# Performance work log

Measured on AMD Instinct MI355X. Metric: run time of the kernel, lower is better.

The kernel has to match this reference:

```python
import jax, jax.numpy as jnp
import numpy as np

N_HEAD = 16
N_KV_HEAD = 4
HEAD_DIM = 64
ROPE_THETA = 10000.0
EPS = 1e-6


def _rope_cos_sin(T, D, theta):
    # matches torch: freqs_cis[t, i] = exp(1j * t * theta**(-2i/D)), i in [0, D//2)
    inv_freq = theta ** (-jnp.arange(0, D, 2, dtype=jnp.float32) / D)  # [D//2]
    freqs = jnp.arange(T, dtype=jnp.float32)[:, None] * inv_freq[None, :]  # [T, D//2]
    return jnp.cos(freqs), jnp.sin(freqs)


def _apply_rope(x, cos, sin):
    # x: [B, T, H, D]; pairs are (even, odd) along last dim, complex-multiplied by freqs_cis
    B, T, H, D = x.shape
    xr = x.reshape(B, T, H, D // 2, 2)
    xe, xo = xr[..., 0], xr[..., 1]
    c = cos[None, :, None, :]  # [1, T, 1, D//2]
    s = sin[None, :, None, :]
    oe = xe * c - xo * s
    oo = xe * s + xo * c
    return jnp.stack([oe, oo], axis=-1).reshape(B, T, H, D)


def _qk_norm(x):
    rms = jnp.sqrt(jnp.mean(x * x, axis=-1, keepdims=True) + EPS)
    return x / rms


def setup_inputs() -> dict:
    key = jax.random.key(0)
    k = jax.random.split(key, 5)
    B, T, C = 4, 2048, 1024
    sc = 1.0 / np.sqrt(C)
    return {
        "x": jax.random.normal(k[0], (B, T, C), jnp.float32),
        "wq": jax.random.normal(k[1], (N_HEAD * HEAD_DIM, C), jnp.float32) * sc,
        "wk": jax.random.normal(k[2], (N_KV_HEAD * HEAD_DIM, C), jnp.float32) * sc,
        "wv": jax.random.normal(k[3], (N_KV_HEAD * HEAD_DIM, C), jnp.float32) * sc,
        "wo": jax.random.normal(k[4], (C, N_HEAD * HEAD_DIM), jnp.float32) * sc,
    }


def reference(x, wq, wk, wv, wo):
    B, T, C = x.shape
    H, KVH, D = N_HEAD, N_KV_HEAD, HEAD_DIM
    n_rep = H // KVH

    q = (x @ wq.T).reshape(B, T, H, D)
    k = (x @ wk.T).reshape(B, T, KVH, D)
    v = (x @ wv.T).reshape(B, T, KVH, D)

    cos, sin = _rope_cos_sin(T, D, ROPE_THETA)
    q = _qk_norm(_apply_rope(q, cos, sin))
    k = _qk_norm(_apply_rope(k, cos, sin))

    # GQA expand kv heads to n_head
    k = jnp.repeat(k, n_rep, axis=2)  # [B, T, H, D]
    v = jnp.repeat(v, n_rep, axis=2)

    q = q.transpose(0, 2, 1, 3)  # [B, H, T, D]
    k = k.transpose(0, 2, 1, 3)
    v = v.transpose(0, 2, 1, 3)

    scale = 1.0 / np.sqrt(D)
    scores = jnp.einsum("bhqd,bhkd->bhqk", q, k) * scale
    causal = jnp.tril(jnp.ones((T, T), dtype=bool))
    scores = jnp.where(causal[None, None], scores, -jnp.inf)
    attn = jax.nn.softmax(scores, axis=-1)
    y = jnp.einsum("bhqk,bhkd->bhqd", attn, v)  # [B, H, T, D]
    y = y.transpose(0, 2, 1, 3).reshape(B, T, H * D)
    return y @ wo.T
```

## Files before the change

kernel.cpp:

```cpp
#include <hip/hip_runtime.h>
#include <hip/hip_bf16.h>
#include <type_traits>

typedef __attribute__((ext_vector_type(8))) __bf16 bf16x8;
typedef __attribute__((ext_vector_type(2))) float f32x2;
typedef __attribute__((ext_vector_type(4))) float f32x4;
typedef __attribute__((ext_vector_type(16))) float f32x16;

#define MFMA16(a, b, c) __builtin_amdgcn_mfma_f32_16x16x32_bf16((a), (b), (c), 0, 0, 0)
#define MFMA32(a, b, c) __builtin_amdgcn_mfma_f32_32x32x16_bf16((a), (b), (c), 0, 0, 0)

__device__ __forceinline__ unsigned short f2bf(float f) {
    unsigned u = __builtin_bit_cast(unsigned, f);
    u = (u + 0x7fffu + ((u >> 16) & 1u)) >> 16;
    return (unsigned short)u;
}

__device__ __forceinline__ float bf2f(unsigned short u) {
    return __builtin_bit_cast(float, (unsigned)u << 16);
}

__device__ __forceinline__ unsigned cvt_pk_bf16(float lo, float hi) {
    unsigned r;
    asm("v_cvt_pk_bf16_f32 %0, %1, %2" : "=v"(r) : "v"(lo), "v"(hi));
    return r;
}

__device__ __forceinline__ void permswap(unsigned& a, unsigned& b) {
    asm("v_permlane32_swap_b32 %0, %1" : "+v"(a), "+v"(b));
}

__device__ __forceinline__ void gll16(const void* g, void* l) {
    __builtin_amdgcn_global_load_lds((const __attribute__((address_space(1))) void*)g,
                                     (__attribute__((address_space(3))) void*)l, 16, 0, 0);
}

__global__ __launch_bounds__(256) void cvt_fused(const float4* __restrict__ x,
                                                 const float4* __restrict__ wq,
                                                 const float4* __restrict__ wk,
                                                 const float4* __restrict__ wv,
                                                 const float4* __restrict__ wo,
                                                 ushort4* __restrict__ xb,
                                                 ushort4* __restrict__ wqkvb,
                                                 ushort4* __restrict__ wob,
                                                 float2* __restrict__ tbl) {
    int i = blockIdx.x * 256 + threadIdx.x;
    if (i < 2752512) {
        const float4* src; ushort4* dst; int j;
        if (i < 2097152)      { src = x;  dst = xb;             j = i; }
        else if (i < 2359296) { src = wq; dst = wqkvb;          j = i - 2097152; }
        else if (i < 2424832) { src = wk; dst = wqkvb + 262144; j = i - 2359296; }
        else if (i < 2490368) { src = wv; dst = wqkvb + 327680; j = i - 2424832; }
        else                  { src = wo; dst = wob;            j = i - 2490368; }
        float4 v = src[j];
        ushort4 o;
        o.x = f2bf(v.x); o.y = f2bf(v.y); o.z = f2bf(v.z); o.w = f2bf(v.w);
        dst[j] = o;
    } else {
        int j = i - 2752512;
        int t = j >> 5, k = j & 31;
        float inv = powf(10000.0f, -(float)(2 * k) * (1.0f / 64.0f));
        float a = (float)t * inv;
        tbl[j] = make_float2(cosf(a), sinf(a));
    }
}

template <typename OT>
__global__ __launch_bounds__(256) void gemm_bt_t(const unsigned short* __restrict__ A,
                                                 const unsigned short* __restrict__ Bt,
                                                 OT* __restrict__ C, int M, int N, int K) {
    __shared__ unsigned short As[2][128 * 32];
    __shared__ unsigned short Bs[2][128 * 32];
    const int tid = threadIdx.x;
    const int wid = tid >> 6, lane = tid & 63;
    const size_t brow = (size_t)blockIdx.x * 128, bcol = (size_t)blockIdx.y * 128;
    const int nkt = K >> 5;

    auto stage = [&](int buf, int kt) {
#pragma unroll
        for (int j = 0; j < 2; ++j) {
            int e = (j * 256 + tid) * 8;
            int r = e >> 5, c = e & 31;
            gll16(A + (brow + r) * K + kt * 32 + c, &As[buf][e]);
        }
#pragma unroll
        for (int j = 0; j < 2; ++j) {
            int e = (j * 256 + tid) * 8;
            int r = e >> 5, c = e & 31;
            gll16(Bt + (bcol + r) * K + kt * 32 + c, &Bs[buf][e]);
        }
    };

    f32x4 acc[4][4] = {};
    const int wm = (wid >> 1) * 64, wn = (wid & 1) * 64;
    const int fr = lane & 15, fk = (lane >> 4) * 8;

    stage(0, 0);
    for (int kt = 0; kt < nkt; ++kt) {
        __syncthreads();
        if (kt + 1 < nkt) stage((kt + 1) & 1, kt + 1);
        const int buf = kt & 1;
        bf16x8 af[4], bfr[4];
#pragma unroll
        for (int i = 0; i < 4; ++i)
            af[i] = *(const bf16x8*)&As[buf][(wm + i * 16 + fr) * 32 + fk];
#pragma unroll
        for (int i = 0; i < 4; ++i)
            bfr[i] = *(const bf16x8*)&Bs[buf][(wn + i * 16 + fr) * 32 + fk];
#pragma unroll
        for (int i = 0; i < 4; ++i)
#pragma unroll
            for (int j = 0; j < 4; ++j)
                acc[i][j] = MFMA16(af[i], bfr[j], acc[i][j]);
    }

    const int orow = (lane >> 4) * 4, ocol = lane & 15;
#pragma unroll
    for (int i = 0; i < 4; ++i)
#pragma unroll
        for (int j = 0; j < 4; ++j)
#pragma unroll
            for (int r = 0; r < 4; ++r) {
                size_t idx = (brow + wm + i * 16 + orow + r) * N + (bcol + wn + j * 16 + ocol);
                if constexpr (std::is_same_v<OT, unsigned short>)
                    C[idx] = f2bf(acc[i][j][r]);
                else
                    C[idx] = acc[i][j][r];
            }
}

__global__ __launch_bounds__(256) void rope_norm(const unsigned short* __restrict__ qkvb,
                                                 const float2* __restrict__ tbl,
                                                 unsigned short* __restrict__ qb,
                                                 unsigned short* __restrict__ kb) {
    int unit = blockIdx.x * 4 + (threadIdx.x >> 6);
    int lane = threadIdx.x & 63;
    int row = unit / 20;
    int hh = unit - row * 20;
    int b = row >> 11, t = row & 2047;
    int col = (hh < 16) ? hh * 64 : 1024 + (hh - 16) * 64;
    float x = bf2f(qkvb[(size_t)row * 1536 + col + lane]);
    float partner = __shfl_xor(x, 1);
    float2 cs = tbl[t * 32 + (lane >> 1)];
    float sgn = (lane & 1) ? cs.y : -cs.y;
    float o = x * cs.x + partner * sgn;
    float ss = o * o;
#pragma unroll
    for (int off = 1; off < 64; off <<= 1) ss += __shfl_xor(ss, off);
    o = o * rsqrtf(ss * (1.0f / 64.0f) + 1e-6f);
    if (hh < 16) o *= 0.18033688f;
    unsigned short ob = f2bf(o);
    if (hh < 16)
        qb[(((size_t)(b * 16 + hh)) * 2048 + t) * 64 + lane] = ob;
    else
        kb[(((size_t)(b * 4 + (hh - 16))) * 2048 + t) * 64 + lane] = ob;
}

__global__ __launch_bounds__(256) void vtrans(const unsigned short* __restrict__ qkvb,
                                              unsigned short* __restrict__ vt) {
    __shared__ unsigned short tile[64][72];
    int bk = blockIdx.y, t0 = blockIdx.x * 64;
    int b = bk >> 2, kvh = bk & 3;
    int i = threadIdx.x >> 2, c0 = (threadIdx.x & 3) * 16;
    const unsigned short* src = qkvb + ((size_t)(b * 2048 + t0)) * 1536 + 1280 + kvh * 64;
#pragma unroll
    for (int j = 0; j < 16; ++j) tile[i][c0 + j] = src[(size_t)i * 1536 + c0 + j];
    __syncthreads();
    unsigned short* dst = vt + (size_t)bk * 64 * 2048 + (size_t)i * 2048 + t0 + c0;
#pragma unroll
    for (int j = 0; j < 16; ++j) dst[j] = tile[c0 + j][i];
}

__global__ __launch_bounds__(256, 4) void attn_fwd(const unsigned short* __restrict__ qb,
                                                   const unsigned short* __restrict__ kbuf,
                                                   const unsigned short* __restrict__ vt,
                                                   unsigned short* __restrict__ Pp,
                                                   float* __restrict__ Lp) {
    int orig = blockIdx.x;
    int wg = (orig & 7) * 320 + (orig >> 3);
    int bh = wg / 40;
    int u = 39 - (wg - bh * 40);
    int qt, ci, nc;
    if (u < 4)       { qt = u;               ci = 0;            nc = 1; }
    else if (u < 12) { qt = 4 + ((u - 4) >> 1);  ci = (u - 4) & 1;  nc = 2; }
    else if (u < 24) { qt = 8 + (u - 12) / 3;    ci = (u - 12) % 3; nc = 3; }
    else             { qt = 12 + ((u - 24) >> 2); ci = (u - 24) & 3; nc = 4; }
    const int nkt = 2 * qt + 2;
    const int t0 = ci * nkt / nc, t1 = (ci + 1) * nkt / nc;
    const int qbase = qt * 128;

    int b = bh >> 4, h = bh & 15, kvh = h >> 2;
    int tid = threadIdx.x, wid = tid >> 6, lane = tid & 63;
    int qrow0 = qbase + wid * 32;
    const unsigned short* Q = qb + ((size_t)(b * 16 + h)) * 2048 * 64;
    const unsigned short* Kp = kbuf + ((size_t)(b * 4 + kvh)) * 2048 * 64;
    const unsigned short* Vp = vt + ((size_t)(b * 4 + kvh)) * 64 * 2048;
    const int q32 = lane & 31, hi = lane >> 5;
    const int swz = (q32 & 7) ^ ((q32 >> 3) & 3);

    __shared__ unsigned short Klds[2][4096];
    __shared__ unsigned short Vlds[2][4096];

    auto stage = [&](int buf, int kt) {
#pragma unroll
        for (int j = 0; j < 2; ++j) {
            int t = j * 256 + tid;
            int k = t >> 3, c = (t & 7) ^ (k & 7) ^ ((k >> 3) & 3);
            gll16(Kp + ((size_t)(kt * 64 + k)) * 64 + c * 8, &Klds[buf][t * 8]);
        }
#pragma unroll
        for (int j = 0; j < 2; ++j) {
            int t = j * 256 + tid;
            int d = t >> 3, c = (t & 7) ^ (d & 7) ^ ((d >> 3) & 3);
            gll16(Vp + (size_t)d * 2048 + kt * 64 + c * 8, &Vlds[buf][t * 8]);
        }
    };

    bf16x8 qf[4];
#pragma unroll
    for (int kd = 0; kd < 4; ++kd)
        qf[kd] = *(const bf16x8*)&Q[(qrow0 + q32) * 64 + kd * 16 + hi * 8];

    f32x16 accO[2] = {};
    f32x2 lr2 = {0.0f, 0.0f};
    f32x16 s0v;
#pragma unroll
    for (int i = 0; i < 16; ++i) s0v[i] = -11.54156036f;

    stage(0, t0);
    for (int kt = t0; kt < t1; ++kt) {
        __syncthreads();
        if (kt + 1 < t1) stage((kt + 1 - t0) & 1, kt + 1);
        const int cur = (kt - t0) & 1;
        const int kb0 = kt * 64;
        if (kb0 <= qrow0 + 31) {
            const int qg = qrow0 + q32;
            const bool diag = (kb0 + 63 > qrow0);
            bf16x8 pf[4];
#pragma unroll
            for (int j = 0; j < 2; ++j) {
                f32x16 s = s0v;
                const int row = j * 32 + q32;
                __builtin_amdgcn_s_setprio(1);
#pragma unroll
                for (int kd = 0; kd < 4; ++kd) {
                    bf16x8 kf = *(const bf16x8*)&Klds[cur][row * 64 + ((2 * kd + hi) ^ swz) * 8];
                    s = MFMA32(kf, qf[kd], s);
                }
                __builtin_amdgcn_s_setprio(0);
                float p[16];
                if (diag) {
#pragma unroll
                    for (int r = 0; r < 16; ++r) {
                        float v = __builtin_exp2f(s[r]);
                        int key = kb0 + j * 32 + (r & 3) + 8 * (r >> 2) + 4 * hi;
                        if (key > qg) v = 0.0f;
                        p[r] = v;
                    }
                } else {
#pragma unroll
                    for (int r = 0; r < 16; ++r) p[r] = __builtin_exp2f(s[r]);
                }
#pragma unroll
                for (int i = 0; i < 8; ++i) {
                    f32x2 pp = {p[2 * i], p[2 * i + 1]};
                    asm("v_pk_add_f32 %0, %0, %1" : "+v"(lr2) : "v"(pp));
                }
#pragma unroll
                for (int kl = 0; kl < 2; ++kl) {
                    unsigned c0 = cvt_pk_bf16(p[8 * kl + 0], p[8 * kl + 1]);
                    unsigned c1 = cvt_pk_bf16(p[8 * kl + 4], p[8 * kl + 5]);
                    unsigned c2 = cvt_pk_bf16(p[8 * kl + 2], p[8 * kl + 3]);
                    unsigned c3 = cvt_pk_bf16(p[8 * kl + 6], p[8 * kl + 7]);
                    permswap(c0, c1);
                    permswap(c2, c3);
                    union { bf16x8 v; unsigned u[4]; } pk;
                    pk.u[0] = c0; pk.u[1] = c2; pk.u[2] = c1; pk.u[3] = c3;
                    pf[j * 2 + kl] = pk.v;
                }
            }
            __builtin_amdgcn_s_setprio(1);
#pragma unroll
            for (int nd = 0; nd < 2; ++nd) {
                int row = nd * 32 + q32;
#pragma unroll
                for (int ks = 0; ks < 4; ++ks) {
                    bf16x8 vf = *(const bf16x8*)&Vlds[cur][row * 64 + ((2 * ks + hi) ^ swz) * 8];
                    accO[nd] = MFMA32(pf[ks], vf, accO[nd]);
                }
            }
            __builtin_amdgcn_s_setprio(0);
        }
    }

    float lrun = lr2[0] + lr2[1];
    unsigned lu = __builtin_bit_cast(unsigned, lrun);
    unsigned la = lu, lb = lu;
    permswap(la, lb);
    float L = __builtin_bit_cast(float, la) + __builtin_bit_cast(float, lb);

    unsigned short* Pw = Pp + (((size_t)bh * 40 + u) * 128 + wid * 32) * 64;
#pragma unroll
    for (int nd = 0; nd < 2; ++nd)
#pragma unroll
        for (int r = 0; r < 16; ++r) {
            int lrow = (r & 3) + 8 * (r >> 2) + 4 * hi;
            Pw[(size_t)lrow * 64 + nd * 32 + q32] = f2bf(accO[nd][r]);
        }
    if (lane < 32)
        Lp[((size_t)bh * 40 + u) * 128 + wid * 32 + q32] = L;
}

__global__ __launch_bounds__(256) void attn_fin(const unsigned short* __restrict__ Pp,
                                                const float* __restrict__ Lp,
                                                unsigned short* __restrict__ y) {
    int idx = blockIdx.x * 256 + threadIdx.x;
    int dg = idx & 15;
    int grow = idx >> 4;
    int bh = grow >> 11, t = grow & 2047;
    int b = bh >> 4, h = bh & 15;
    int qt = t >> 7;
    int bse, nc;
    if (qt < 4)       { bse = qt;                nc = 1; }
    else if (qt < 8)  { bse = 4 + 2 * (qt - 4);  nc = 2; }
    else if (qt < 12) { bse = 12 + 3 * (qt - 8); nc = 3; }
    else              { bse = 24 + 4 * (qt - 12); nc = 4; }
    float o0 = 0.f, o1 = 0.f, o2 = 0.f, o3 = 0.f, L = 0.f;
    for (int ci = 0; ci < nc; ++ci) {
        size_t slot = ((size_t)bh * 40 + bse + ci) * 128 + (t & 127);
        ushort4 pw = *(const ushort4*)&Pp[slot * 64 + dg * 4];
        o0 += bf2f(pw.x); o1 += bf2f(pw.y); o2 += bf2f(pw.z); o3 += bf2f(pw.w);
        L += Lp[slot];
    }
    float inv = 1.0f / L;
    ushort4 w;
    w.x = f2bf(o0 * inv); w.y = f2bf(o1 * inv);
    w.z = f2bf(o2 * inv); w.w = f2bf(o3 * inv);
    *(ushort4*)&y[((size_t)(b * 2048 + t)) * 1024 + h * 64 + dg * 4] = w;
}

extern "C" void kernel_launch(void* const* d_in, const int* in_sizes, int n_in,
                              void* d_out, int out_size, void* d_ws, size_t ws_size,
                              hipStream_t stream) {
    const float* x = (const float*)d_in[0];
    const float* wq = (const float*)d_in[1];
    const float* wk = (const float*)d_in[2];
    const float* wv = (const float*)d_in[3];
    const float* wo = (const float*)d_in[4];
    float* out = (float*)d_out;

    char* ws = (char*)d_ws;
    size_t off = 0;
    auto alloc = [&](size_t bytes) {
        void* p = ws + off;
        off += (bytes + 255) & ~(size_t)255;
        return p;
    };
    unsigned short* xb    = (unsigned short*)alloc(8192ull * 1024 * 2);
    unsigned short* wqkvb = (unsigned short*)alloc(1536ull * 1024 * 2);
    unsigned short* wob   = (unsigned short*)alloc(1024ull * 1024 * 2);
    char*           big   = (char*)alloc(41943040ull + 1310720ull);
    float2*         tbl   = (float2*)alloc(2048ull * 32 * 8);
    unsigned short* qb    = (unsigned short*)alloc(8192ull * 1024 * 2);
    unsigned short* kb    = (unsigned short*)alloc(4ull * 4 * 2048 * 64 * 2);
    unsigned short* vt    = (unsigned short*)alloc(4ull * 4 * 64 * 2048 * 2);

    unsigned short* qkvb  = (unsigned short*)big;
    unsigned short* Pp    = (unsigned short*)big;
    float*          Lp    = (float*)(big + 41943040ull);
    unsigned short* ybf   = xb;

    cvt_fused<<<11008, 256, 0, stream>>>((const float4*)x, (const float4*)wq, (const float4*)wk,
                                         (const float4*)wv, (const float4*)wo,
                                         (ushort4*)xb, (ushort4*)wqkvb, (ushort4*)wob, tbl);

    gemm_bt_t<unsigned short><<<dim3(64, 12), 256, 0, stream>>>(xb, wqkvb, qkvb, 8192, 1536, 1024);

    rope_norm<<<(8192 * 20) / 4, 256, 0, stream>>>(qkvb, tbl, qb, kb);

    vtrans<<<dim3(32, 16), 256, 0, stream>>>(qkvb, vt);

    attn_fwd<<<2560, 256, 0, stream>>>(qb, kb, vt, Pp, Lp);

    attn_fin<<<8192, 256, 0, stream>>>(Pp, Lp, ybf);

    gemm_bt_t<float><<<dim3(64, 8), 256, 0, stream>>>(ybf, wob, out, 8192, 1024, 1024);
}
```

Baseline: 174.8 us.

## Fuse RoPE, QK-norm and V transpose into QKV GEMM epilogue

Adds a QKV GEMM whose epilogue applies rotary embedding and RMS normalisation in registers and writes Q/K in head-major layout and V transposed. This removes the rope_norm and vtrans kernels and the round trip of the intermediate qkv buffer through memory. Separately, attention staging now precomputes and increments global pointers instead of recomputing addresses, and the row-sum accumulation is split into four independent accumulators to shorten the dependency chain. The epilogue issues many per-element table loads and shuffles and uses scattered 2-byte stores, which may be less coalesced than before.

Result: no change. 174.2 us, median of 4 (-0.4%).

```diff
diff --git a/kernel.cpp b/kernel.cpp
--- a/kernel.cpp
+++ b/kernel.cpp
@@ -65,6 +65,127 @@
     }
 }
 
+__global__ __launch_bounds__(256) void gemm_qkv(const unsigned short* __restrict__ A,
+                                                const unsigned short* __restrict__ Bt,
+                                                const float2* __restrict__ tbl,
+                                                unsigned short* __restrict__ qb,
+                                                unsigned short* __restrict__ kb,
+                                                unsigned short* __restrict__ vt) {
+    const int K = 1024;
+    __shared__ unsigned short As[2][128 * 32];
+    __shared__ unsigned short Bs[2][128 * 32];
+    const int tid = threadIdx.x;
+    const int wid = tid >> 6, lane = tid & 63;
+    const size_t brow = (size_t)blockIdx.x * 128, bcol = (size_t)blockIdx.y * 128;
+    const int nkt = K >> 5;
+
+    auto stage = [&](int buf, int kt) {
+#pragma unroll
+        for (int j = 0; j < 2; ++j) {
+            int e = (j * 256 + tid) * 8;
+            int r = e >> 5, c = e & 31;
+            gll16(A + (brow + r) * K + kt * 32 + c, &As[buf][e]);
+        }
+#pragma unroll
+        for (int j = 0; j < 2; ++j) {
+            int e = (j * 256 + tid) * 8;
+            int r = e >> 5, c = e & 31;
+            gll16(Bt + (bcol + r) * K + kt * 32 + c, &Bs[buf][e]);
+        }
+    };
+
+    f32x4 acc[4][4] = {};
+    const int wm = (wid >> 1) * 64, wn = (wid & 1) * 64;
+    const int fr = lane & 15, fk = (lane >> 4) * 8;
+
+    stage(0, 0);
+    for (int kt = 0; kt < nkt; ++kt) {
+        __syncthreads();
+        if (kt + 1 < nkt) stage((kt + 1) & 1, kt + 1);
+        const int buf = kt & 1;
+        bf16x8 af[4], bfr[4];
+#pragma unroll
+        for (int i = 0; i < 4; ++i)
+            af[i] = *(const bf16x8*)&As[buf][(wm + i * 16 + fr) * 32 + fk];
+#pragma unroll
+        for (int i = 0; i < 4; ++i)
+            bfr[i] = *(const bf16x8*)&Bs[buf][(wn + i * 16 + fr) * 32 + fk];
+#pragma unroll
+        for (int i = 0; i < 4; ++i)
+#pragma unroll
+            for (int j = 0; j < 4; ++j)
+                acc[i][j] = MFMA16(af[i], bfr[j], acc[i][j]);
+    }
+
+    const int orow = (lane >> 4) * 4, ocol = lane & 15;
+    const int tokrow0 = (int)brow + wm;
+    const int hcol0 = (int)bcol + wn;
+
+    if (blockIdx.y < 10) {
+        float ss[4][4];
+#pragma unroll
+        for (int i = 0; i < 4; ++i)
+#pragma unroll
+            for (int r = 0; r < 4; ++r) ss[i][r] = 0.0f;
+#pragma unroll
+        for (int i = 0; i < 4; ++i)
+#pragma unroll
+            for (int j = 0; j < 4; ++j) {
+                const int m = (j * 16 + ocol) >> 1;
+#pragma unroll
+                for (int r = 0; r < 4; ++r) {
+                    float xv = acc[i][j][r];
+                    float partner = __shfl_xor(xv, 1);
+                    int t = (tokrow0 + i * 16 + orow + r) & 2047;
+                    float2 cs = tbl[t * 32 + m];
+                    float sgn = (ocol & 1) ? cs.y : -cs.y;
+                    float v = fmaf(xv, cs.x, partner * sgn);
+                    acc[i][j][r] = v;
+                    ss[i][r] += v * v;
+                }
+            }
+#pragma unroll
+        for (int off = 1; off < 16; off <<= 1)
+#pragma unroll
+            for (int i = 0; i < 4; ++i)
+#pragma unroll
+                for (int r = 0; r < 4; ++r) ss[i][r] += __shfl_xor(ss[i][r], off);
+        const bool isq = (blockIdx.y < 8);
+        const float qsc = isq ? 0.18033688f : 1.0f;
+        const int h = hcol0 >> 6;
+#pragma unroll
+        for (int i = 0; i < 4; ++i)
+#pragma unroll
+            for (int r = 0; r < 4; ++r) {
+                float sc = rsqrtf(ss[i][r] * (1.0f / 64.0f) + 1e-6f) * qsc;
+                int grow = tokrow0 + i * 16 + orow + r;
+                int b = grow >> 11, t = grow & 2047;
+                unsigned short* dst = isq
+                    ? qb + (((size_t)(b * 16 + h)) * 2048 + t) * 64
+                    : kb + (((size_t)(b * 4 + (h - 16))) * 2048 + t) * 64;
+#pragma unroll
+                for (int j = 0; j < 4; ++j)
+                    dst[j * 16 + ocol] = f2bf(acc[i][j][r] * sc);
+            }
+    } else {
+#pragma unroll
+        for (int j = 0; j < 4; ++j) {
+            int vcol = (hcol0 - 1280) + j * 16 + ocol;
+            int kvh = vcol >> 6, d = vcol & 63;
+#pragma unroll
+            for (int i = 0; i < 4; ++i) {
+                int grow = tokrow0 + i * 16 + orow;
+                int b = grow >> 11, t = grow & 2047;
+                ushort4 w;
+#pragma unroll
+                for (int r = 0; r < 4; ++r)
+                    ((unsigned short*)&w)[r] = f2bf(acc[i][j][r]);
+                *(ushort4*)&vt[((size_t)(b * 4 + kvh) * 64 + d) * 2048 + t] = w;
+            }
+        }
+    }
+}
+
 template <typename OT>
 __global__ __launch_bounds__(256) void gemm_bt_t(const unsigned short* __restrict__ A,
                                                  const unsigned short* __restrict__ Bt,
@@ -127,48 +248,6 @@
                 else
                     C[idx] = acc[i][j][r];
             }
-}
-
-__global__ __launch_bounds__(256) void rope_norm(const unsigned short* __restrict__ qkvb,
-                                                 const float2* __restrict__ tbl,
-                                                 unsigned short* __restrict__ qb,
-                                                 unsigned short* __restrict__ kb) {
-    int unit = blockIdx.x * 4 + (threadIdx.x >> 6);
-    int lane = threadIdx.x & 63;
-    int row = unit / 20;
-    int hh = unit - row * 20;
-    int b = row >> 11, t = row & 2047;
-    int col = (hh < 16) ? hh * 64 : 1024 + (hh - 16) * 64;
-    float x = bf2f(qkvb[(size_t)row * 1536 + col + lane]);
-    float partner = __shfl_xor(x, 1);
-    float2 cs = tbl[t * 32 + (lane >> 1)];
-    float sgn = (lane & 1) ? cs.y : -cs.y;
-    float o = x * cs.x + partner * sgn;
-    float ss = o * o;
-#pragma unroll
-    for (int off = 1; off < 64; off <<= 1) ss += __shfl_xor(ss, off);
-    o = o * rsqrtf(ss * (1.0f / 64.0f) + 1e-6f);
-    if (hh < 16) o *= 0.18033688f;
-    unsigned short ob = f2bf(o);
-    if (hh < 16)
-        qb[(((size_t)(b * 16 + hh)) * 2048 + t) * 64 + lane] = ob;
-    else
-        kb[(((size_t)(b * 4 + (hh - 16))) * 2048 + t) * 64 + lane] = ob;
-}
-
-__global__ __launch_bounds__(256) void vtrans(const unsigned short* __restrict__ qkvb,
-                                              unsigned short* __restrict__ vt) {
-    __shared__ unsigned short tile[64][72];
-    int bk = blockIdx.y, t0 = blockIdx.x * 64;
-    int b = bk >> 2, kvh = bk & 3;
-    int i = threadIdx.x >> 2, c0 = (threadIdx.x & 3) * 16;
-    const unsigned short* src = qkvb + ((size_t)(b * 2048 + t0)) * 1536 + 1280 + kvh * 64;
-#pragma unroll
-    for (int j = 0; j < 16; ++j) tile[i][c0 + j] = src[(size_t)i * 1536 + c0 + j];
-    __syncthreads();
-    unsigned short* dst = vt + (size_t)bk * 64 * 2048 + (size_t)i * 2048 + t0 + c0;
-#pragma unroll
-    for (int j = 0; j < 16; ++j) dst[j] = tile[c0 + j][i];
 }
 
 __global__ __launch_bounds__(256, 4) void attn_fwd(const unsigned short* __restrict__ qb,
@@ -201,19 +280,22 @@
     __shared__ unsigned short Klds[2][4096];
     __shared__ unsigned short Vlds[2][4096];
 
-    auto stage = [&](int buf, int kt) {
-#pragma unroll
-        for (int j = 0; j < 2; ++j) {
-            int t = j * 256 + tid;
-            int k = t >> 3, c = (t & 7) ^ (k & 7) ^ ((k >> 3) & 3);
-            gll16(Kp + ((size_t)(kt * 64 + k)) * 64 + c * 8, &Klds[buf][t * 8]);
-        }
-#pragma unroll
-        for (int j = 0; j < 2; ++j) {
-            int t = j * 256 + tid;
-            int d = t >> 3, c = (t & 7) ^ (d & 7) ^ ((d >> 3) & 3);
-            gll16(Vp + (size_t)d * 2048 + kt * 64 + c * 8, &Vlds[buf][t * 8]);
-        }
+    const unsigned short *gk0, *gk1, *gv0, *gv1;
+    {
+        int t = tid, k = t >> 3, c = (t & 7) ^ (k & 7) ^ ((k >> 3) & 3);
+        gk0 = Kp + ((size_t)(t0 * 64 + k)) * 64 + c * 8;
+        t = 256 + tid; k = t >> 3; c = (t & 7) ^ (k & 7) ^ ((k >> 3) & 3);
+        gk1 = Kp + ((size_t)(t0 * 64 + k)) * 64 + c * 8;
+        t = tid; int d = t >> 3; c = (t & 7) ^ (d & 7) ^ ((d >> 3) & 3);
+        gv0 = Vp + (size_t)d * 2048 + t0 * 64 + c * 8;
+        t = 256 + tid; d = t >> 3; c = (t & 7) ^ (d & 7) ^ ((d >> 3) & 3);
+        gv1 = Vp + (size_t)d * 2048 + t0 * 64 + c * 8;
+    }
+    auto stage = [&](int buf) {
+        gll16(gk0, &Klds[buf][tid * 8]);        gk0 += 4096;
+        gll16(gk1, &Klds[buf][2048 + tid * 8]); gk1 += 4096;
+        gll16(gv0, &Vlds[buf][tid * 8]);        gv0 += 64;
+        gll16(gv1, &Vlds[buf][2048 + tid * 8]); gv1 += 64;
     };
 
     bf16x8 qf[4];
@@ -222,15 +304,15 @@
         qf[kd] = *(const bf16x8*)&Q[(qrow0 + q32) * 64 + kd * 16 + hi * 8];
 
     f32x16 accO[2] = {};
-    f32x2 lr2 = {0.0f, 0.0f};
+    f32x2 lra = {0.0f, 0.0f}, lrb = {0.0f, 0.0f}, lrc = {0.0f, 0.0f}, lrd = {0.0f, 0.0f};
     f32x16 s0v;
 #pragma unroll
     for (int i = 0; i < 16; ++i) s0v[i] = -11.54156036f;
 
-    stage(0, t0);
+    stage(0);
     for (int kt = t0; kt < t1; ++kt) {
         __syncthreads();
-        if (kt + 1 < t1) stage((kt + 1 - t0) & 1, kt + 1);
+        if (kt + 1 < t1) stage((kt + 1 - t0) & 1);
         const int cur = (kt - t0) & 1;
         const int kb0 = kt * 64;
         if (kb0 <= qrow0 + 31) {
@@ -261,10 +343,19 @@
 #pragma unroll
                     for (int r = 0; r < 16; ++r) p[r] = __builtin_exp2f(s[r]);
                 }
-#pragma unroll
-                for (int i = 0; i < 8; ++i) {
-                    f32x2 pp = {p[2 * i], p[2 * i + 1]};
-                    asm("v_pk_add_f32 %0, %0, %1" : "+v"(lr2) : "v"(pp));
+                {
+                    f32x2 p0 = {p[0], p[1]},  p1 = {p[2], p[3]};
+                    f32x2 p2 = {p[4], p[5]},  p3 = {p[6], p[7]};
+                    asm("v_pk_add_f32 %0, %0, %1" : "+v"(lra) : "v"(p0));
+                    asm("v_pk_add_f32 %0, %0, %1" : "+v"(lrb) : "v"(p1));
+                    asm("v_pk_add_f32 %0, %0, %1" : "+v"(lrc) : "v"(p2));
+                    asm("v_pk_add_f32 %0, %0, %1" : "+v"(lrd) : "v"(p3));
+                    f32x2 p4 = {p[8], p[9]},  p5 = {p[10], p[11]};
+                    f32x2 p6 = {p[12], p[13]}, p7 = {p[14], p[15]};
+                    asm("v_pk_add_f32 %0, %0, %1" : "+v"(lra) : "v"(p4));
+                    asm("v_pk_add_f32 %0, %0, %1" : "+v"(lrb) : "v"(p5));
+                    asm("v_pk_add_f32 %0, %0, %1" : "+v"(lrc) : "v"(p6));
+                    asm("v_pk_add_f32 %0, %0, %1" : "+v"(lrd) : "v"(p7));
                 }
 #pragma unroll
                 for (int kl = 0; kl < 2; ++kl) {
@@ -293,7 +384,10 @@
         }
     }
 
-    float lrun = lr2[0] + lr2[1];
+    asm("v_pk_add_f32 %0, %0, %1" : "+v"(lra) : "v"(lrc));
+    asm("v_pk_add_f32 %0, %0, %1" : "+v"(lrb) : "v"(lrd));
+    asm("v_pk_add_f32 %0, %0, %1" : "+v"(lra) : "v"(lrb));
+    float lrun = lra[0] + lra[1];
     unsigned lu = __builtin_bit_cast(unsigned, lrun);
     unsigned la = lu, lb = lu;
     permswap(la, lb);
@@ -359,26 +453,19 @@
     unsigned short* xb    = (unsigned short*)alloc(8192ull * 1024 * 2);
     unsigned short* wqkvb = (unsigned short*)alloc(1536ull * 1024 * 2);
     unsigned short* wob   = (unsigned short*)alloc(1024ull * 1024 * 2);
-    char*           big   = (char*)alloc(41943040ull + 1310720ull);
+    unsigned short* Pp    = (unsigned short*)alloc(41943040ull);
+    float*          Lp    = (float*)alloc(1310720ull);
     float2*         tbl   = (float2*)alloc(2048ull * 32 * 8);
     unsigned short* qb    = (unsigned short*)alloc(8192ull * 1024 * 2);
     unsigned short* kb    = (unsigned short*)alloc(4ull * 4 * 2048 * 64 * 2);
     unsigned short* vt    = (unsigned short*)alloc(4ull * 4 * 64 * 2048 * 2);
-
-    unsigned short* qkvb  = (unsigned short*)big;
-    unsigned short* Pp    = (unsigned short*)big;
-    float*          Lp    = (float*)(big + 41943040ull);
     unsigned short* ybf   = xb;
 
     cvt_fused<<<11008, 256, 0, stream>>>((const float4*)x, (const float4*)wq, (const float4*)wk,
                                          (const float4*)wv, (const float4*)wo,
                                          (ushort4*)xb, (ushort4*)wqkvb, (ushort4*)wob, tbl);
 
-    gemm_bt_t<unsigned short><<<dim3(64, 12), 256, 0, stream>>>(xb, wqkvb, qkvb, 8192, 1536, 1024);
-
-    rope_norm<<<(8192 * 20) / 4, 256, 0, stream>>>(qkvb, tbl, qb, kb);
-
-    vtrans<<<dim3(32, 16), 256, 0, stream>>>(qkvb, vt);
+    gemm_qkv<<<dim3(64, 12), 256, 0, stream>>>(xb, wqkvb, tbl, qb, kb, vt);
 
     attn_fwd<<<2560, 256, 0, stream>>>(qb, kb, vt, Pp, Lp);
 
```
